# Kernel tuning notes

Measured on AMD Instinct MI355X. Metric: run time of the kernel, lower is better.

Reference implementation:

```python
import jax, jax.numpy as jnp
import numpy as np

E = 30000          # nEdges
K_PER_EDGE = 12    # quadruplets per edge
KMAX = 16          # padded K dimension
Q = E * K_PER_EDGE # nQuadruplets = 360000
I = 180000         # intermediate (db) expansion size
DE, DQ, DB = 128, 64, 64   # emb_size_edge, emb_size_quad, emb_size_bilinear
DRBF, DCBF, DSBF = 16, 16, 32
NSPH = 32
SCALE_SILU = 1.0 / 0.6


def _act(x):
    # GemNet ScaledSiLU
    return jax.nn.silu(x) * SCALE_SILU


def setup_inputs() -> dict:
    key = jax.random.key(0)
    ks = jax.random.split(key, 16)
    inp = {}
    inp["m"] = jax.random.normal(ks[0], (E, DE), jnp.float32)
    inp["rbf"] = jax.random.normal(ks[1], (E, DRBF), jnp.float32)
    inp["cbf"] = jax.random.normal(ks[2], (I, DCBF), jnp.float32)
    inp["sbf_W1"] = jax.random.normal(ks[3], (E, DSBF, NSPH), jnp.float32) * 0.1
    inp["sph"] = jax.random.normal(ks[4], (E, KMAX, NSPH), jnp.float32) * 0.1
    # structured, valid scatter indices: 12 distinct K-slots per edge
    inp["Kidx4"] = jnp.tile(jnp.arange(K_PER_EDGE, dtype=jnp.int32), E)
    inp["id4_reduce_ca"] = jnp.repeat(jnp.arange(E, dtype=jnp.int32), K_PER_EDGE)
    inp["id_swap"] = jax.random.permutation(ks[5], E).astype(jnp.int32)
    inp["id4_expand_intm_db"] = jax.random.randint(ks[6], (I,), 0, E, jnp.int32)
    inp["id4_expand_abd"] = jax.random.randint(ks[7], (Q,), 0, I, jnp.int32)
    # parameters (bias-free Dense layers + bilinear weight + scaling factors)
    def w(k, shape, fan_in):
        return jax.random.normal(k, shape, jnp.float32) / np.sqrt(fan_in)
    inp["W_db"] = w(ks[8], (DE, DE), DE)
    inp["W_rbf"] = w(ks[9], (DRBF, DE), DRBF)
    inp["W_down"] = w(ks[10], (DE, DQ), DE)
    inp["W_cbf"] = w(ks[11], (DCBF, DQ), DCBF)
    inp["W_bilin"] = w(ks[12], (DQ, DSBF, DB), DQ * DSBF)
    inp["W_up_ca"] = w(ks[13], (DB, DE), DB)
    inp["W_up_ac"] = w(ks[14], (DB, DE), DB)
    inp["s_rbf"] = jnp.asarray(1.1, jnp.float32)
    inp["s_cbf"] = jnp.asarray(0.9, jnp.float32)
    inp["s_sbf"] = jnp.asarray(1.2, jnp.float32)
    return inp


def reference(m, rbf, cbf, sbf_W1, sph,
              W_db, W_rbf, W_down, W_cbf, W_bilin, W_up_ca, W_up_ac,
              s_rbf, s_cbf, s_sbf,
              Kidx4, id_swap, id4_reduce_ca, id4_expand_intm_db, id4_expand_abd):
    # dense_db + hadamard with rbf MLP + scale
    x_db = _act(m @ W_db)                        # (E, DE)
    x_db = (x_db * (rbf @ W_rbf)) * s_rbf        # scale_rbf scales the product
    # down projection to quad size, expand to intermediate set
    x_db = _act(x_db @ W_down)                   # (E, DQ)
    x_db = x_db[id4_expand_intm_db]              # (I, DQ)
    # hadamard with cbf MLP + scale, expand to quadruplets
    x_db = (x_db * (cbf @ W_cbf)) * s_cbf        # (I, DQ)
    x_db = x_db[id4_expand_abd]                  # (Q, DQ)
    # EfficientInteractionBilinear: scatter quads into padded (E, Kmax, DQ)
    m2 = jnp.zeros((E, KMAX, DQ), x_db.dtype).at[id4_reduce_ca, Kidx4].set(x_db)
    sum_k = jnp.einsum("eks,ekq->esq", sph, m2)          # (E, NSPH, DQ)
    rw = jnp.einsum("eis,esq->eiq", sbf_W1, sum_k)       # (E, DSBF, DQ)
    x = jnp.einsum("eiq,qib->eb", rw, W_bilin)           # (E, DB)
    x = x * s_sbf                                         # scale_sbf_sum
    # up projections; swap directions for ac
    x_ca = _act(x @ W_up_ca)                     # (E, DE)
    x_ac = _act(x @ W_up_ac)[id_swap]            # (E, DE)
    return (x_ca + x_ac) * (1.0 / np.sqrt(2.0))
```

## Files before the change

kernel.cpp:

```cpp
#include <hip/hip_runtime.h>
#include <hip/hip_bf16.h>


#define E_N   30000
#define KPE   12
#define KMAXX 16
#define I_N   180000
#define DE    128
#define DQ    64
#define DB    64
#define DRBF  16
#define DCBF  16
#define DSBF  32
#define NSPH  32
#define SCALE_SILU (1.0f/0.6f)
#define INV_SQRT2  0.70710678118654752f

typedef __attribute__((ext_vector_type(8))) short bf16x8;
typedef __attribute__((ext_vector_type(4))) float f32x4;

__device__ __forceinline__ float silu_scaled(float x) {
    return x / (1.0f + __expf(-x)) * SCALE_SILU;
}

__device__ __forceinline__ short f2bf(float x) {
    unsigned u = __float_as_uint(x);
    u += 0x7fffu + ((u >> 16) & 1u);
    return (short)(u >> 16);
}
__device__ __forceinline__ float bf2f(ushort u) {
    return __uint_as_float(((unsigned)u) << 16);
}

__device__ __forceinline__ bf16x8 cvt8(const float4 a, const float4 b) {
    bf16x8 t;
    t[0]=f2bf(a.x); t[1]=f2bf(a.y); t[2]=f2bf(a.z); t[3]=f2bf(a.w);
    t[4]=f2bf(b.x); t[5]=f2bf(b.y); t[6]=f2bf(b.z); t[7]=f2bf(b.w);
    return t;
}

#define PK_WDBT   0
#define PK_WRBFT  16384
#define PK_WDOWNT 20480
#define PK_WUPAT  28672
#define PK_WUPBT  36864
#define PK_BT     45056
#define PK_TOTAL  176128

__global__ __launch_bounds__(256) void kw_prep(
    const float* __restrict__ Wdb, const float* __restrict__ Wrbf,
    const float* __restrict__ Wdown, const float* __restrict__ WupA,
    const float* __restrict__ WupB, const float* __restrict__ Wbil,
    ushort* __restrict__ wpk)
{
    const int idx = blockIdx.x * 256 + threadIdx.x;
    float v;
    if (idx < PK_WRBFT) {
        const int n = idx >> 7, k = idx & 127;
        v = Wdb[k * DE + n];
    } else if (idx < PK_WDOWNT) {
        const int j = idx - PK_WRBFT;
        const int n = j >> 5, k = j & 31;
        v = (k < DRBF) ? Wrbf[k * DE + n] : 0.f;
    } else if (idx < PK_WUPAT) {
        const int j = idx - PK_WDOWNT;
        const int q = j >> 7, k = j & 127;
        v = Wdown[k * DQ + q];
    } else if (idx < PK_WUPBT) {
        const int j = idx - PK_WUPAT;
        const int d = j >> 6, b = j & 63;
        v = WupA[b * DE + d];
    } else if (idx < PK_BT) {
        const int j = idx - PK_WUPBT;
        const int d = j >> 6, b = j & 63;
        v = WupB[b * DE + d];
    } else {
        const int j = idx - PK_BT;
        const int b = j >> 11, jj = j & 2047;
        const int i = jj >> 6, q = jj & 63;
        v = Wbil[(size_t)(q * DSBF + i) * DB + b];
    }
    wpk[idx] = (ushort)f2bf(v);
}

__global__ __launch_bounds__(256) void k1_mfma(
    const float* __restrict__ m, const float* __restrict__ rbf,
    const ushort* __restrict__ wpk, const float* __restrict__ s_rbf_p,
    ushort* __restrict__ Tb)
{
    const int l  = threadIdx.x & 63;
    const int wv = __builtin_amdgcn_readfirstlane(threadIdx.x >> 6);
    const int e0 = (blockIdx.x * 4 + wv) * 16;
    if (e0 >= E_N) return;
    const int mr = l & 15;
    const int kg = l >> 4;
    const ushort* WdbT  = wpk + PK_WDBT;
    const ushort* WrbfT = wpk + PK_WRBFT;

    f32x4 accH[8], accR[8];
    #pragma unroll
    for (int nt = 0; nt < 8; ++nt)
        #pragma unroll
        for (int r = 0; r < 4; ++r) { accH[nt][r] = 0.f; accR[nt][r] = 0.f; }

    bf16x8 ra;
    if (kg < 2) {
        const float* rr = rbf + (size_t)(e0 + mr) * DRBF + kg * 8;
        ra = cvt8(*(const float4*)rr, *(const float4*)(rr + 4));
    } else {
        #pragma unroll
        for (int j = 0; j < 8; ++j) ra[j] = 0;
    }
    #pragma unroll
    for (int nt = 0; nt < 8; ++nt) {
        const bf16x8 rb = *(const bf16x8*)(WrbfT + (nt*16 + mr)*32 + kg*8);
        accR[nt] = __builtin_amdgcn_mfma_f32_16x16x32_bf16(ra, rb, accR[nt], 0,0,0);
    }

    const float* mrow = m + (size_t)(e0 + mr) * DE + kg * 8;
    #pragma unroll
    for (int kt = 0; kt < 4; ++kt) {
        const float* ms = mrow + kt * 32;
        const bf16x8 a = cvt8(*(const float4*)ms, *(const float4*)(ms + 4));
        #pragma unroll
        for (int nt = 0; nt < 8; ++nt) {
            const bf16x8 b = *(const bf16x8*)(WdbT + (nt*16 + mr)*128 + kt*32 + kg*8);
            accH[nt] = __builtin_amdgcn_mfma_f32_16x16x32_bf16(a, b, accH[nt], 0,0,0);
        }
    }

    const float srbf = s_rbf_p[0];
    ushort* tout = Tb + (size_t)(e0 + kg*4) * DE + mr;
    #pragma unroll
    for (int nt = 0; nt < 8; ++nt)
        #pragma unroll
        for (int r = 0; r < 4; ++r)
            tout[(size_t)r * DE + 16*nt] =
                (ushort)f2bf(silu_scaled(accH[nt][r]) * accR[nt][r] * srbf);
}

__global__ __launch_bounds__(256) void k1b_mfma(
    const ushort* __restrict__ Tb, const ushort* __restrict__ wpk,
    float* __restrict__ xq)
{
    const int l  = threadIdx.x & 63;
    const int wv = __builtin_amdgcn_readfirstlane(threadIdx.x >> 6);
    const int e0 = (blockIdx.x * 4 + wv) * 16;
    if (e0 >= E_N) return;
    const int mr = l & 15;
    const int kg = l >> 4;
    const ushort* WdownT = wpk + PK_WDOWNT;

    f32x4 acc[4];
    #pragma unroll
    for (int nt = 0; nt < 4; ++nt)
        #pragma unroll
        for (int r = 0; r < 4; ++r) acc[nt][r] = 0.f;

    const ushort* arow = Tb + (size_t)(e0 + mr) * DE + kg * 8;
    #pragma unroll
    for (int kt = 0; kt < 4; ++kt) {
        const bf16x8 a = *(const bf16x8*)(arow + kt * 32);
        #pragma unroll
        for (int nt = 0; nt < 4; ++nt) {
            const bf16x8 b = *(const bf16x8*)(WdownT + (nt*16 + mr)*128 + kt*32 + kg*8);
            acc[nt] = __builtin_amdgcn_mfma_f32_16x16x32_bf16(a, b, acc[nt], 0,0,0);
        }
    }
    float* xout = xq + (size_t)(e0 + kg*4) * DQ + mr;
    #pragma unroll
    for (int nt = 0; nt < 4; ++nt)
        #pragma unroll
        for (int r = 0; r < 4; ++r)
            xout[(size_t)r * DQ + 16*nt] = silu_scaled(acc[nt][r]);
}

__global__ __launch_bounds__(256) void k2_intm(
    const float* __restrict__ cbf, const int* __restrict__ idx_db,
    const float* __restrict__ xq, const float* __restrict__ Wcbf,
    const float* __restrict__ s_cbf_p, ushort* __restrict__ y)
{
    __shared__ float sW[DCBF*DQ];
    for (int i = threadIdx.x; i < DCBF*DQ; i += 256) sW[i] = Wcbf[i];
    __syncthreads();
    const float sc = s_cbf_p[0];
    const int lane = threadIdx.x & 63;
    const int wv = __builtin_amdgcn_readfirstlane(threadIdx.x >> 6);
    for (int row = blockIdx.x*4 + wv; row < I_N; row += gridDim.x*4) {
        const float* cr = cbf + (size_t)row*DCBF;
        float acc = 0.f;
        #pragma unroll
        for (int k = 0; k < DCBF; ++k) acc += cr[k] * sW[k*DQ + lane];
        const int src = idx_db[row];
        y[(size_t)row*DQ + lane] =
            (ushort)f2bf(xq[(size_t)src*DQ + lane] * acc * sc);
    }
}

__global__ __launch_bounds__(256, 4) void k3_fused(
    const ushort* __restrict__ y, const float* __restrict__ sph,
    const float* __restrict__ sbf, const int* __restrict__ kidx,
    const int* __restrict__ abd, const ushort* __restrict__ wpk,
    const float* __restrict__ s_sbf_p, ushort* __restrict__ Xb)
{
    __shared__ ushort sRw[8 * 2048];
    const int l  = threadIdx.x & 63;
    const int wv = __builtin_amdgcn_readfirstlane(threadIdx.x >> 6);
    const int e0 = blockIdx.x * 8;
    const int q0 = l & 15;
    const int sg = l >> 4;
    const int s0 = sg * 8;

    for (int ei = 0; ei < 2; ++ei) {
        const int eL = wv * 2 + ei;
        const int e  = e0 + eL;

        float SK[8][4];
        #pragma unroll
        for (int r = 0; r < 8; ++r)
            #pragma unroll
            for (int c = 0; c < 4; ++c) SK[r][c] = 0.f;

        const int base = e * KPE;
        #pragma unroll
        for (int j = 0; j < KPE; ++j) {
            const int kj = kidx[base + j];
            const int aj = abd[base + j];
            const ushort* yr = y + (size_t)aj * DQ;
            const float v0 = bf2f(yr[q0]);
            const float v1 = bf2f(yr[q0 + 16]);
            const float v2 = bf2f(yr[q0 + 32]);
            const float v3 = bf2f(yr[q0 + 48]);
            const float* sp = sph + ((size_t)e * KMAXX + kj) * NSPH + s0;
            const float4 sA = *(const float4*)sp;
            const float4 sB = *(const float4*)(sp + 4);
            const float sv[8] = {sA.x, sA.y, sA.z, sA.w, sB.x, sB.y, sB.z, sB.w};
            #pragma unroll
            for (int r = 0; r < 8; ++r) {
                SK[r][0] = __builtin_fmaf(sv[r], v0, SK[r][0]);
                SK[r][1] = __builtin_fmaf(sv[r], v1, SK[r][1]);
                SK[r][2] = __builtin_fmaf(sv[r], v2, SK[r][2]);
                SK[r][3] = __builtin_fmaf(sv[r], v3, SK[r][3]);
            }
        }

        bf16x8 bfrag[4];
        #pragma unroll
        for (int qt = 0; qt < 4; ++qt) {
            bf16x8 t;
            #pragma unroll
            for (int r = 0; r < 8; ++r) t[r] = f2bf(SK[r][qt]);
            bfrag[qt] = t;
        }

        const float* sb0 = sbf + ((size_t)e * DSBF + q0) * NSPH + s0;
        bf16x8 afrag[2];
        #pragma unroll
        for (int h = 0; h < 2; ++h) {
            const float* ar = sb0 + h * 16 * NSPH;
            afrag[h] = cvt8(*(const float4*)ar, *(const float4*)(ar + 4));
        }

        f32x4 acc[2][4];
        #pragma unroll
        for (int h = 0; h < 2; ++h)
            #pragma unroll
            for (int qt = 0; qt < 4; ++qt)
                #pragma unroll
                for (int r = 0; r < 4; ++r) acc[h][qt][r] = 0.f;

        #pragma unroll
        for (int h = 0; h < 2; ++h)
            #pragma unroll
            for (int qt = 0; qt < 4; ++qt)
                acc[h][qt] = __builtin_amdgcn_mfma_f32_16x16x32_bf16(
                    afrag[h], bfrag[qt], acc[h][qt], 0, 0, 0);

        ushort* ro = sRw + eL * 2048;
        #pragma unroll
        for (int h = 0; h < 2; ++h)
            #pragma unroll
            for (int r = 0; r < 4; ++r) {
                const int i = h * 16 + sg * 4 + r;
                #pragma unroll
                for (int qt = 0; qt < 4; ++qt) {
                    const int f = i * DQ + q0 + 16 * qt;
                    ro[f ^ (sg << 4) ^ (eL << 3)] = (ushort)f2bf(acc[h][qt][r]);
                }
            }
    }
    __syncthreads();

    const int eA  = l & 7;
    const int kg  = l >> 4;
    const ushort* brow = wpk + PK_BT + (size_t)(wv * 16 + (l & 15)) * 2048 + kg * 8;
    const ushort* arow = sRw + eA * 2048;

    f32x4 xacc;
    #pragma unroll
    for (int r = 0; r < 4; ++r) xacc[r] = 0.f;

    #pragma unroll 8
    for (int kt = 0; kt < 64; ++kt) {
        const int f0 = kt * 32 + kg * 8;
        const int S0 = f0 ^ ((((unsigned)kt >> 3) & 3) << 4) ^ (eA << 3);
        const bf16x8 a = *(const bf16x8*)(arow + S0);
        const bf16x8 b = *(const bf16x8*)(brow + kt * 32);
        xacc = __builtin_amdgcn_mfma_f32_16x16x32_bf16(a, b, xacc, 0, 0, 0);
    }

    const float ss = s_sbf_p[0];
    if (sg < 2) {
        ushort* xout = Xb + (size_t)(e0 + sg * 4) * DQ + wv * 16 + (l & 15);
        #pragma unroll
        for (int r = 0; r < 4; ++r)
            xout[(size_t)r * DQ] = (ushort)f2bf(xacc[r] * ss);
    }
}

__global__ __launch_bounds__(256) void k4_mfma(
    const ushort* __restrict__ Xb, const ushort* __restrict__ wpk,
    ushort* __restrict__ Abh, ushort* __restrict__ Bbh)
{
    const int l  = threadIdx.x & 63;
    const int wv = __builtin_amdgcn_readfirstlane(threadIdx.x >> 6);
    const int e0 = (blockIdx.x * 4 + wv) * 16;
    if (e0 >= E_N) return;
    const int mr = l & 15;
    const int kg = l >> 4;
    const ushort* WupAT = wpk + PK_WUPAT;
    const ushort* WupBT = wpk + PK_WUPBT;

    f32x4 accA[8], accB[8];
    #pragma unroll
    for (int nt = 0; nt < 8; ++nt)
        #pragma unroll
        for (int r = 0; r < 4; ++r) { accA[nt][r] = 0.f; accB[nt][r] = 0.f; }

    const ushort* arow = Xb + (size_t)(e0 + mr) * DQ + kg * 8;
    #pragma unroll
    for (int kt = 0; kt < 2; ++kt) {
        const bf16x8 a = *(const bf16x8*)(arow + kt * 32);
        #pragma unroll
        for (int nt = 0; nt < 8; ++nt) {
            const bf16x8 bA = *(const bf16x8*)(WupAT + (nt*16 + mr)*64 + kt*32 + kg*8);
            accA[nt] = __builtin_amdgcn_mfma_f32_16x16x32_bf16(a, bA, accA[nt], 0,0,0);
            const bf16x8 bB = *(const bf16x8*)(WupBT + (nt*16 + mr)*64 + kt*32 + kg*8);
            accB[nt] = __builtin_amdgcn_mfma_f32_16x16x32_bf16(a, bB, accB[nt], 0,0,0);
        }
    }
    ushort* aout = Abh + (size_t)(e0 + kg*4) * DE + mr;
    ushort* bout = Bbh + (size_t)(e0 + kg*4) * DE + mr;
    #pragma unroll
    for (int nt = 0; nt < 8; ++nt)
        #pragma unroll
        for (int r = 0; r < 4; ++r) {
            aout[(size_t)r * DE + 16*nt] = (ushort)f2bf(silu_scaled(accA[nt][r]));
            bout[(size_t)r * DE + 16*nt] = (ushort)f2bf(silu_scaled(accB[nt][r]));
        }
}

__global__ __launch_bounds__(256) void k5_comb(
    const ushort* __restrict__ Abh, const ushort* __restrict__ Bbh,
    const int* __restrict__ swp, float* __restrict__ out)
{
    const int i8   = blockIdx.x*256 + threadIdx.x;
    const int flat = i8*8;
    const int e = flat >> 7;
    const int d = flat & 127;
    const bf16x8 a = *(const bf16x8*)(Abh + flat);
    const int es = swp[e];
    const bf16x8 b = *(const bf16x8*)(Bbh + (size_t)es*DE + d);
    float4 o0, o1;
    o0.x = (bf2f((ushort)a[0]) + bf2f((ushort)b[0])) * INV_SQRT2;
    o0.y = (bf2f((ushort)a[1]) + bf2f((ushort)b[1])) * INV_SQRT2;
    o0.z = (bf2f((ushort)a[2]) + bf2f((ushort)b[2])) * INV_SQRT2;
    o0.w = (bf2f((ushort)a[3]) + bf2f((ushort)b[3])) * INV_SQRT2;
    o1.x = (bf2f((ushort)a[4]) + bf2f((ushort)b[4])) * INV_SQRT2;
    o1.y = (bf2f((ushort)a[5]) + bf2f((ushort)b[5])) * INV_SQRT2;
    o1.z = (bf2f((ushort)a[6]) + bf2f((ushort)b[6])) * INV_SQRT2;
    o1.w = (bf2f((ushort)a[7]) + bf2f((ushort)b[7])) * INV_SQRT2;
    *(float4*)(out + flat)     = o0;
    *(float4*)(out + flat + 4) = o1;
}

extern "C" void kernel_launch(void* const* d_in, const int* in_sizes, int n_in,
                              void* d_out, int out_size, void* d_ws, size_t ws_size,
                              hipStream_t stream)
{
    const float* m      = (const float*)d_in[0];
    const float* rbf    = (const float*)d_in[1];
    const float* cbf    = (const float*)d_in[2];
    const float* sbfW1  = (const float*)d_in[3];
    const float* sph    = (const float*)d_in[4];
    const int*   kidx   = (const int*)d_in[5];
    const int*   idswap = (const int*)d_in[7];
    const int*   idin   = (const int*)d_in[8];
    const int*   abd    = (const int*)d_in[9];
    const float* Wdb    = (const float*)d_in[10];
    const float* Wrbf   = (const float*)d_in[11];
    const float* Wdown  = (const float*)d_in[12];
    const float* Wcbf   = (const float*)d_in[13];
    const float* Wbil   = (const float*)d_in[14];
    const float* WupA   = (const float*)d_in[15];
    const float* WupB   = (const float*)d_in[16];
    const float* s_rbf  = (const float*)d_in[17];
    const float* s_cbf  = (const float*)d_in[18];
    const float* s_sbf  = (const float*)d_in[19];
    float* out = (float*)d_out;

    float* ws   = (float*)d_ws;
    ushort* Tb  = (ushort*)ws;
    float*  xq  = ws +  1920000;
    ushort* y   = (ushort*)(ws + 3840000);
    ushort* Xb  = (ushort*)(ws + 9600000);
    ushort* Abh = (ushort*)(ws + 10560000);
    ushort* Bbh = (ushort*)(ws + 12480000);
    ushort* wpk = (ushort*)(ws + 14400000);

    kw_prep  <<<688,  256, 0, stream>>>(Wdb, Wrbf, Wdown, WupA, WupB, Wbil, wpk);
    k1_mfma  <<<469,  256, 0, stream>>>(m, rbf, wpk, s_rbf, Tb);
    k1b_mfma <<<469,  256, 0, stream>>>(Tb, wpk, xq);
    k2_intm  <<<1024, 256, 0, stream>>>(cbf, idin, xq, Wcbf, s_cbf, y);
    k3_fused <<<3750, 256, 0, stream>>>(y, sph, sbfW1, kidx, abd, wpk, s_sbf, Xb);
    k4_mfma  <<<469,  256, 0, stream>>>(Xb, wpk, Abh, Bbh);
    k5_comb  <<<1875, 256, 0, stream>>>(Abh, Bbh, idswap, out);
}
```

Baseline: 517.4 us.

## Store xq in bf16, vectorize y gathers, transpose bilinear MFMA, split accumulators

```diff
diff --git a/kernel.cpp b/kernel.cpp
--- a/kernel.cpp
+++ b/kernel.cpp
@@ -30,6 +30,9 @@
 }
 __device__ __forceinline__ float bf2f(ushort u) {
     return __uint_as_float(((unsigned)u) << 16);
+}
+__device__ __forceinline__ unsigned pk2(float a, float b) {
+    return (unsigned)(ushort)f2bf(a) | ((unsigned)(ushort)f2bf(b) << 16);
 }
 
 __device__ __forceinline__ bf16x8 cvt8(const float4 a, const float4 b) {
@@ -77,7 +80,8 @@
     } else {
         const int j = idx - PK_BT;
         const int b = j >> 11, jj = j & 2047;
-        const int i = jj >> 6, q = jj & 63;
+        const int i = jj >> 6, vq = jj & 63;
+        const int q = 4 * (vq & 15) + (vq >> 4);
         v = Wbil[(size_t)(q * DSBF + i) * DB + b];
     }
     wpk[idx] = (ushort)f2bf(v);
@@ -141,7 +145,7 @@
 
 __global__ __launch_bounds__(256) void k1b_mfma(
     const ushort* __restrict__ Tb, const ushort* __restrict__ wpk,
-    float* __restrict__ xq)
+    ushort* __restrict__ xqb)
 {
     const int l  = threadIdx.x & 63;
     const int wv = __builtin_amdgcn_readfirstlane(threadIdx.x >> 6);
@@ -167,17 +171,17 @@
             acc[nt] = __builtin_amdgcn_mfma_f32_16x16x32_bf16(a, b, acc[nt], 0,0,0);
         }
     }
-    float* xout = xq + (size_t)(e0 + kg*4) * DQ + mr;
+    ushort* xout = xqb + (size_t)(e0 + kg*4) * DQ + mr;
     #pragma unroll
     for (int nt = 0; nt < 4; ++nt)
         #pragma unroll
         for (int r = 0; r < 4; ++r)
-            xout[(size_t)r * DQ + 16*nt] = silu_scaled(acc[nt][r]);
+            xout[(size_t)r * DQ + 16*nt] = (ushort)f2bf(silu_scaled(acc[nt][r]));
 }
 
 __global__ __launch_bounds__(256) void k2_intm(
     const float* __restrict__ cbf, const int* __restrict__ idx_db,
-    const float* __restrict__ xq, const float* __restrict__ Wcbf,
+    const ushort* __restrict__ xqb, const float* __restrict__ Wcbf,
     const float* __restrict__ s_cbf_p, ushort* __restrict__ y)
 {
     __shared__ float sW[DCBF*DQ];
@@ -193,7 +197,7 @@
         for (int k = 0; k < DCBF; ++k) acc += cr[k] * sW[k*DQ + lane];
         const int src = idx_db[row];
         y[(size_t)row*DQ + lane] =
-            (ushort)f2bf(xq[(size_t)src*DQ + lane] * acc * sc);
+            (ushort)f2bf(bf2f(xqb[(size_t)src*DQ + lane]) * acc * sc);
     }
 }
 
@@ -207,7 +211,7 @@
     const int l  = threadIdx.x & 63;
     const int wv = __builtin_amdgcn_readfirstlane(threadIdx.x >> 6);
     const int e0 = blockIdx.x * 8;
-    const int q0 = l & 15;
+    const int c  = l & 15;
     const int sg = l >> 4;
     const int s0 = sg * 8;
 
@@ -219,18 +223,18 @@
         #pragma unroll
         for (int r = 0; r < 8; ++r)
             #pragma unroll
-            for (int c = 0; c < 4; ++c) SK[r][c] = 0.f;
+            for (int q = 0; q < 4; ++q) SK[r][q] = 0.f;
 
         const int base = e * KPE;
         #pragma unroll
         for (int j = 0; j < KPE; ++j) {
             const int kj = kidx[base + j];
             const int aj = abd[base + j];
-            const ushort* yr = y + (size_t)aj * DQ;
-            const float v0 = bf2f(yr[q0]);
-            const float v1 = bf2f(yr[q0 + 16]);
-            const float v2 = bf2f(yr[q0 + 32]);
-            const float v3 = bf2f(yr[q0 + 48]);
+            const uint2 yv = *(const uint2*)(y + (size_t)aj * DQ + 4*c);
+            const float v0 = bf2f((ushort)(yv.x & 0xffffu));
+            const float v1 = bf2f((ushort)(yv.x >> 16));
+            const float v2 = bf2f((ushort)(yv.y & 0xffffu));
+            const float v3 = bf2f((ushort)(yv.y >> 16));
             const float* sp = sph + ((size_t)e * KMAXX + kj) * NSPH + s0;
             const float4 sA = *(const float4*)sp;
             const float4 sB = *(const float4*)(sp + 4);
@@ -244,74 +248,81 @@
             }
         }
 
-        bf16x8 bfrag[4];
+        bf16x8 af[4];
         #pragma unroll
         for (int qt = 0; qt < 4; ++qt) {
             bf16x8 t;
             #pragma unroll
             for (int r = 0; r < 8; ++r) t[r] = f2bf(SK[r][qt]);
-            bfrag[qt] = t;
-        }
-
-        const float* sb0 = sbf + ((size_t)e * DSBF + q0) * NSPH + s0;
-        bf16x8 afrag[2];
+            af[qt] = t;
+        }
+
+        const float* sb0 = sbf + ((size_t)e * DSBF + c) * NSPH + s0;
+        bf16x8 bfg[2];
         #pragma unroll
         for (int h = 0; h < 2; ++h) {
             const float* ar = sb0 + h * 16 * NSPH;
-            afrag[h] = cvt8(*(const float4*)ar, *(const float4*)(ar + 4));
-        }
-
-        f32x4 acc[2][4];
+            bfg[h] = cvt8(*(const float4*)ar, *(const float4*)(ar + 4));
+        }
+
+        f32x4 accT[4][2];
+        #pragma unroll
+        for (int qt = 0; qt < 4; ++qt)
+            #pragma unroll
+            for (int h = 0; h < 2; ++h)
+                #pragma unroll
+                for (int r = 0; r < 4; ++r) accT[qt][h][r] = 0.f;
+
+        #pragma unroll
+        for (int qt = 0; qt < 4; ++qt)
+            #pragma unroll
+            for (int h = 0; h < 2; ++h)
+                accT[qt][h] = __builtin_amdgcn_mfma_f32_16x16x32_bf16(
+                    af[qt], bfg[h], accT[qt][h], 0, 0, 0);
+
+        ushort* ro = sRw + eL * 2048;
+        const int swz = ((c & 7) << 3) ^ ((eL & 7) << 3);
         #pragma unroll
         for (int h = 0; h < 2; ++h)
             #pragma unroll
-            for (int qt = 0; qt < 4; ++qt)
-                #pragma unroll
-                for (int r = 0; r < 4; ++r) acc[h][qt][r] = 0.f;
-
-        #pragma unroll
-        for (int h = 0; h < 2; ++h)
-            #pragma unroll
-            for (int qt = 0; qt < 4; ++qt)
-                acc[h][qt] = __builtin_amdgcn_mfma_f32_16x16x32_bf16(
-                    afrag[h], bfrag[qt], acc[h][qt], 0, 0, 0);
-
-        ushort* ro = sRw + eL * 2048;
-        #pragma unroll
-        for (int h = 0; h < 2; ++h)
-            #pragma unroll
-            for (int r = 0; r < 4; ++r) {
-                const int i = h * 16 + sg * 4 + r;
-                #pragma unroll
-                for (int qt = 0; qt < 4; ++qt) {
-                    const int f = i * DQ + q0 + 16 * qt;
-                    ro[f ^ (sg << 4) ^ (eL << 3)] = (ushort)f2bf(acc[h][qt][r]);
-                }
+            for (int qt = 0; qt < 4; ++qt) {
+                uint2 w;
+                w.x = pk2(accT[qt][h][0], accT[qt][h][1]);
+                w.y = pk2(accT[qt][h][2], accT[qt][h][3]);
+                const int jb = 1024*h + 64*c + 16*qt + 4*sg;
+                *(uint2*)(ro + (jb ^ swz)) = w;
             }
     }
     __syncthreads();
 
     const int eA  = l & 7;
     const int kg  = l >> 4;
-    const ushort* brow = wpk + PK_BT + (size_t)(wv * 16 + (l & 15)) * 2048 + kg * 8;
+    const ushort* brow = wpk + PK_BT + (size_t)(wv * 16 + c) * 2048 + kg * 8;
     const ushort* arow = sRw + eA * 2048;
-
+    const int rsw = (eA & 7) << 3;
+
+    f32x4 xa[4];
+    #pragma unroll
+    for (int t = 0; t < 4; ++t)
+        #pragma unroll
+        for (int r = 0; r < 4; ++r) xa[t][r] = 0.f;
+
+    #pragma unroll 16
+    for (int kt = 0; kt < 64; ++kt) {
+        const int j0 = kt * 32 + kg * 8;
+        const int S  = j0 ^ (((j0 >> 6) & 7) << 3) ^ rsw;
+        const bf16x8 a = *(const bf16x8*)(arow + S);
+        const bf16x8 b = *(const bf16x8*)(brow + kt * 32);
+        xa[kt & 3] = __builtin_amdgcn_mfma_f32_16x16x32_bf16(a, b, xa[kt & 3], 0, 0, 0);
+    }
     f32x4 xacc;
     #pragma unroll
-    for (int r = 0; r < 4; ++r) xacc[r] = 0.f;
-
-    #pragma unroll 8
-    for (int kt = 0; kt < 64; ++kt) {
-        const int f0 = kt * 32 + kg * 8;
-        const int S0 = f0 ^ ((((unsigned)kt >> 3) & 3) << 4) ^ (eA << 3);
-        const bf16x8 a = *(const bf16x8*)(arow + S0);
-        const bf16x8 b = *(const bf16x8*)(brow + kt * 32);
-        xacc = __builtin_amdgcn_mfma_f32_16x16x32_bf16(a, b, xacc, 0, 0, 0);
-    }
+    for (int r = 0; r < 4; ++r)
+        xacc[r] = (xa[0][r] + xa[1][r]) + (xa[2][r] + xa[3][r]);
 
     const float ss = s_sbf_p[0];
     if (sg < 2) {
-        ushort* xout = Xb + (size_t)(e0 + sg * 4) * DQ + wv * 16 + (l & 15);
+        ushort* xout = Xb + (size_t)(e0 + sg * 4) * DQ + wv * 16 + c;
         #pragma unroll
         for (int r = 0; r < 4; ++r)
             xout[(size_t)r * DQ] = (ushort)f2bf(xacc[r] * ss);
@@ -411,17 +422,17 @@
 
     float* ws   = (float*)d_ws;
     ushort* Tb  = (ushort*)ws;
-    float*  xq  = ws +  1920000;
-    ushort* y   = (ushort*)(ws + 3840000);
-    ushort* Xb  = (ushort*)(ws + 9600000);
-    ushort* Abh = (ushort*)(ws + 10560000);
-    ushort* Bbh = (ushort*)(ws + 12480000);
-    ushort* wpk = (ushort*)(ws + 14400000);
+    ushort* xqb = (ushort*)(ws + 1920000);
+    ushort* y   = (ushort*)(ws + 2880000);
+    ushort* Xb  = (ushort*)(ws + 8640000);
+    ushort* Abh = (ushort*)(ws + 9600000);
+    ushort* Bbh = (ushort*)(ws + 11520000);
+    ushort* wpk = (ushort*)(ws + 13440000);
 
     kw_prep  <<<688,  256, 0, stream>>>(Wdb, Wrbf, Wdown, WupA, WupB, Wbil, wpk);
     k1_mfma  <<<469,  256, 0, stream>>>(m, rbf, wpk, s_rbf, Tb);
-    k1b_mfma <<<469,  256, 0, stream>>>(Tb, wpk, xq);
-    k2_intm  <<<1024, 256, 0, stream>>>(cbf, idin, xq, Wcbf, s_cbf, y);
+    k1b_mfma <<<469,  256, 0, stream>>>(Tb, wpk, xqb);
+    k2_intm  <<<2048, 256, 0, stream>>>(cbf, idin, xqb, Wcbf, s_cbf, y);
     k3_fused <<<3750, 256, 0, stream>>>(y, sph, sbfW1, kidx, abd, wpk, s_sbf, Xb);
     k4_mfma  <<<469,  256, 0, stream>>>(Xb, wpk, Abh, Bbh);
     k5_comb  <<<1875, 256, 0, stream>>>(Abh, Bbh, idswap, out);
```

New measurement: 476.0 us. 1.09x faster.
